# Performance work log

Hardware: AMD Instinct MI355X
Metric: run time of the kernel (lower is better)

The kernel has to match this reference:

```python
import jax, jax.numpy as jnp
import numpy as np

LOG_SQRT_2PI = 0.5 * float(np.log(2.0 * np.pi))  # 0.5*log(2*pi)


def _bayes_layer(x, mu, p, eps):
    # std_w = 1e-6 + softplus(W_p); W = W_mu + std_w * eps
    std = 1e-6 + jax.nn.softplus(p)
    W = mu + std * eps
    out = x @ W
    # variational posterior loglike q(W | mu, std), summed
    lqw = jnp.sum(-LOG_SQRT_2PI - jnp.log(std) - 0.5 * ((W - mu) / std) ** 2)
    # prior loglike N(0, 1) on detached W (original does W.detach().cpu().numpy())
    Wd = jax.lax.stop_gradient(W)
    lpw = jnp.sum(-LOG_SQRT_2PI - 0.5 * Wd ** 2)
    return out, lqw, lpw


def setup_inputs() -> dict:
    key = jax.random.key(0)
    ks = jax.random.split(key, 10)
    B, D_in, D_h, D_out = 65536, 512, 512, 10
    u = lambda k, s, lo, hi: jax.random.uniform(k, s, jnp.float32, lo, hi)
    return {
        "x": jax.random.normal(ks[0], (B, D_in), jnp.float32),
        "W_mu1": u(ks[1], (D_in, D_h), -0.2, 0.2),
        "W_p1": u(ks[2], (D_in, D_h), -3.0, -2.0),
        "eps1": jax.random.normal(ks[3], (D_in, D_h), jnp.float32),
        "W_mu2": u(ks[4], (D_h, D_h), -0.2, 0.2),
        "W_p2": u(ks[5], (D_h, D_h), -3.0, -2.0),
        "eps2": jax.random.normal(ks[6], (D_h, D_h), jnp.float32),
        "W_mu3": u(ks[7], (D_h, D_out), -0.2, 0.2),
        "W_p3": u(ks[8], (D_h, D_out), -3.0, -2.0),
        "eps3": jax.random.normal(ks[9], (D_h, D_out), jnp.float32),
    }


def reference(x, W_mu1, W_p1, eps1, W_mu2, W_p2, eps2, W_mu3, W_p3, eps3):
    # training / sample=True path of bayes_linear_2L.forward
    h, lqw1, lpw1 = _bayes_layer(x, W_mu1, W_p1, eps1)
    h = jax.nn.relu(h)
    h, lqw2, lpw2 = _bayes_layer(h, W_mu2, W_p2, eps2)
    h = jax.nn.relu(h)
    y, lqw3, lpw3 = _bayes_layer(h, W_mu3, W_p3, eps3)
    tlqw = lqw1 + lqw2 + lqw3
    tlpw = lpw1 + lpw2 + lpw3
    return (y, tlqw, tlpw)
```

## Files before the change

### kernel.cpp

```cpp
#include <hip/hip_runtime.h>
#include <hip/hip_bf16.h>
#include <stdint.h>

typedef unsigned char u8;
typedef unsigned int u32;
typedef long i64;
typedef i64 i64x2 __attribute__((ext_vector_type(2)));
typedef float f32x4 __attribute__((ext_vector_type(4)));

#define LOGSQRT2PI 0.9189385332046727f
#define SB0() __builtin_amdgcn_sched_barrier(0)
#define MFMA8(A, B, C) __builtin_amdgcn_mfma_f32_16x16x32_fp8_fp8(A, B, C, 0, 0, 0)

__device__ __forceinline__ void gload_lds16(const void* g, void* l) {
    __builtin_amdgcn_global_load_lds((__attribute__((address_space(1))) void*)g,
                                     (__attribute__((address_space(3))) void*)l,
                                     16, 0, 0);
}

__device__ __forceinline__ u8 to_fp8(float v) {
    return (u8)(__builtin_amdgcn_cvt_pk_fp8_f32(v, 0.f, 0, false) & 0xff);
}

__device__ __forceinline__ void prep_body(const float* __restrict__ mu,
        const float* __restrict__ p, const float* __restrict__ eps,
        u8* __restrict__ Wt, int N, int Npad, float* __restrict__ osc,
        int vb, int nblocks) {
    int total = 512 * Npad;
    float lqw = 0.f, lpw = 0.f;
    for (int idx = vb * 256 + threadIdx.x; idx < total; idx += nblocks * 256) {
        int k = idx / Npad, n = idx - k * Npad;
        float w = 0.f;
        if (n < N) {
            int src = k * N + n;
            float m = mu[src], e = eps[src];
            float sd = 1e-6f + log1pf(expf(p[src]));
            w = m + sd * e;
            float z = (w - m) / sd;
            lqw += -LOGSQRT2PI - logf(sd) - 0.5f * z * z;
            lpw += -LOGSQRT2PI - 0.5f * w * w;
        }
        Wt[n * 512 + k] = to_fp8(w);
    }
    #pragma unroll
    for (int off = 32; off; off >>= 1) {
        lqw += __shfl_down(lqw, off);
        lpw += __shfl_down(lpw, off);
    }
    if ((threadIdx.x & 63) == 0) {
        atomicAdd(&osc[0], lqw);
        atomicAdd(&osc[1], lpw);
    }
}

__global__ void k_prep_all(const float* __restrict__ mu1, const float* __restrict__ p1,
                           const float* __restrict__ e1,
                           const float* __restrict__ mu2, const float* __restrict__ p2,
                           const float* __restrict__ e2,
                           const float* __restrict__ mu3, const float* __restrict__ p3,
                           const float* __restrict__ e3,
                           u8* __restrict__ Wt1, u8* __restrict__ Wt2,
                           u8* __restrict__ Wt3, float* __restrict__ osc) {
    int b = blockIdx.x;
    if (b < 256)      prep_body(mu1, p1, e1, Wt1, 512, 512, osc, b, 256);
    else if (b < 512) prep_body(mu2, p2, e2, Wt2, 512, 512, osc, b - 256, 256);
    else              prep_body(mu3, p3, e3, Wt3, 10,  16,  osc, b - 512, 16);
}

__global__ void k_cvt8(const float4* __restrict__ in, uint2* __restrict__ out, int n8) {
    int stride = gridDim.x * blockDim.x;
    for (int i = blockIdx.x * blockDim.x + threadIdx.x; i < n8; i += stride) {
        float4 a = in[2 * i], b = in[2 * i + 1];
        u32 lo = __builtin_amdgcn_cvt_pk_fp8_f32(a.x, a.y, 0, false);
        lo = __builtin_amdgcn_cvt_pk_fp8_f32(a.z, a.w, (int)lo, true);
        u32 hi = __builtin_amdgcn_cvt_pk_fp8_f32(b.x, b.y, 0, false);
        hi = __builtin_amdgcn_cvt_pk_fp8_f32(b.z, b.w, (int)hi, true);
        out[i] = make_uint2(lo, hi);
    }
}

__global__ __launch_bounds__(256, 2)
void k_f8(const u8* __restrict__ xb, const u8* __restrict__ W1t,
          const u8* __restrict__ W2t, const u8* __restrict__ W3t,
          float* __restrict__ Y) {
    __shared__ __align__(16) u8 L[81920];
    const int tid = threadIdx.x;
    const int l = tid & 63, w = tid >> 6;
    const int r = l & 15, kq = l >> 4;
    const int l16 = l * 16;
    const long m0 = (long)blockIdx.x * 128 + w * 32;
    u8* scr = &L[65536 + w * 4096];

    #define STAGEW(WT, NT) { _Pragma("unroll")                                 \
        for (int i = 0; i < 16; i++) {                                         \
            const int c = w * 16 + i;                                          \
            gload_lds16((WT) + ((NT) * 128 + (c & 7) * 16 + r) * 512           \
                              + (c >> 3) * 64 + kq * 16,                       \
                        &L[c * 1024 + l16]);                                   \
        } }

    #define GLOOP(XF, ACC) { _Pragma("unroll")                                 \
        for (int kt = 0; kt < 8; kt++)                                         \
            _Pragma("unroll")                                                  \
            for (int jg = 0; jg < 8; jg++) {                                   \
                i64x2 bfr = *(const i64x2*)&L[(kt * 8 + jg) * 1024 + l16];     \
                ACC[jg] = MFMA8(XF[kt].x, bfr.x, ACC[jg]);                     \
                ACC[jg] = MFMA8(XF[kt].y, bfr.y, ACC[jg]);                     \
            } }

    #define TOSCR(ACC, RH) { _Pragma("unroll")                                 \
        for (int jg = 0; jg < 8; jg++)                                         \
            _Pragma("unroll")                                                  \
            for (int q = 0; q < 4; q++) {                                      \
                int row = (RH) * 16 + kq * 4 + q;                              \
                scr[row * 128 + ((jg ^ (row & 7)) << 4) + r] =                 \
                    to_fp8(fmaxf(ACC[jg][q], 0.f));                            \
            } }

    i64x2 xfA[8], xfB[8];
    #pragma unroll
    for (int kt = 0; kt < 8; kt++) {
        xfA[kt] = *(const i64x2*)(xb + (m0 + r) * 512 + kt * 64 + kq * 16);
        xfB[kt] = *(const i64x2*)(xb + (m0 + 16 + r) * 512 + kt * 64 + kq * 16);
    }

    i64x2 h1fA[8], h1fB[8];
    f32x4 yA = (f32x4){0.f, 0.f, 0.f, 0.f};
    f32x4 yB = (f32x4){0.f, 0.f, 0.f, 0.f};
    f32x4 acc[8];

    #pragma unroll 1
    for (int nt = 0; nt < 4; nt++) {
        STAGEW(W1t, nt);
        asm volatile("s_waitcnt vmcnt(0)" ::: "memory");
        __builtin_amdgcn_s_barrier();
        #pragma unroll
        for (int jg = 0; jg < 8; jg++) acc[jg] = (f32x4){0.f, 0.f, 0.f, 0.f};
        GLOOP(xfA, acc);
        TOSCR(acc, 0);
        #pragma unroll
        for (int jg = 0; jg < 8; jg++) acc[jg] = (f32x4){0.f, 0.f, 0.f, 0.f};
        GLOOP(xfB, acc);
        TOSCR(acc, 1);
        __builtin_amdgcn_s_barrier();
        asm volatile("s_waitcnt lgkmcnt(0)" ::: "memory");
        SB0();
        #pragma unroll
        for (int t2 = 0; t2 < 2; t2++) {
            h1fA[nt * 2 + t2] = *(const i64x2*)
                &scr[r * 128 + (((t2 * 4 + kq) ^ (r & 7)) << 4)];
            h1fB[nt * 2 + t2] = *(const i64x2*)
                &scr[(16 + r) * 128 + (((t2 * 4 + kq) ^ (r & 7)) << 4)];
        }
        asm volatile("s_waitcnt lgkmcnt(0)" ::: "memory");
        SB0();
    }

    #pragma unroll 1
    for (int nt = 0; nt < 4; nt++) {
        STAGEW(W2t, nt);
        asm volatile("s_waitcnt vmcnt(0)" ::: "memory");
        __builtin_amdgcn_s_barrier();
        #pragma unroll
        for (int jg = 0; jg < 8; jg++) acc[jg] = (f32x4){0.f, 0.f, 0.f, 0.f};
        GLOOP(h1fA, acc);
        TOSCR(acc, 0);
        #pragma unroll
        for (int jg = 0; jg < 8; jg++) acc[jg] = (f32x4){0.f, 0.f, 0.f, 0.f};
        GLOOP(h1fB, acc);
        TOSCR(acc, 1);
        __builtin_amdgcn_s_barrier();
        asm volatile("s_waitcnt lgkmcnt(0)" ::: "memory");
        SB0();
        #pragma unroll
        for (int t2 = 0; t2 < 2; t2++) {
            i64x2 a3A = *(const i64x2*)
                &scr[r * 128 + (((t2 * 4 + kq) ^ (r & 7)) << 4)];
            i64x2 a3B = *(const i64x2*)
                &scr[(16 + r) * 128 + (((t2 * 4 + kq) ^ (r & 7)) << 4)];
            i64x2 w3 = *(const i64x2*)(W3t + r * 512 + nt * 128 + t2 * 64 + kq * 16);
            yA = MFMA8(a3A.x, w3.x, yA);
            yA = MFMA8(a3A.y, w3.y, yA);
            yB = MFMA8(a3B.x, w3.x, yB);
            yB = MFMA8(a3B.y, w3.y, yB);
        }
        asm volatile("s_waitcnt lgkmcnt(0)" ::: "memory");
        SB0();
    }

    if (r < 10) {
        #pragma unroll
        for (int q = 0; q < 4; q++) {
            Y[(m0 + kq * 4 + q) * 10 + r]      = yA[q];
            Y[(m0 + 16 + kq * 4 + q) * 10 + r] = yB[q];
        }
    }
    #undef STAGEW
    #undef GLOOP
    #undef TOSCR
}

extern "C" void kernel_launch(void* const* d_in, const int* in_sizes, int n_in,
                              void* d_out, int out_size, void* d_ws, size_t ws_size,
                              hipStream_t stream) {
    const float* x   = (const float*)d_in[0];
    const float* mu1 = (const float*)d_in[1];
    const float* p1  = (const float*)d_in[2];
    const float* e1  = (const float*)d_in[3];
    const float* mu2 = (const float*)d_in[4];
    const float* p2  = (const float*)d_in[5];
    const float* e2  = (const float*)d_in[6];
    const float* mu3 = (const float*)d_in[7];
    const float* p3  = (const float*)d_in[8];
    const float* e3  = (const float*)d_in[9];
    float* out = (float*)d_out;

    const int B = 65536, D = 512, DO = 10;

    char* ws = (char*)d_ws;
    u8* Wt1 = (u8*)(ws);
    u8* Wt2 = (u8*)(ws + 262144);
    u8* Wt3 = (u8*)(ws + 524288);
    u8* xb  = (u8*)(ws + 1048576);

    float* osc = out + (long)B * DO;

    hipMemsetAsync(osc, 0, 2 * sizeof(float), stream);
    hipLaunchKernelGGL(k_prep_all, dim3(528), dim3(256), 0, stream,
                       mu1, p1, e1, mu2, p2, e2, mu3, p3, e3, Wt1, Wt2, Wt3, osc);
    hipLaunchKernelGGL(k_cvt8, dim3(2048), dim3(256), 0, stream,
                       (const float4*)x, (uint2*)xb, B * D / 8);
    hipLaunchKernelGGL(k_f8, dim3(512), dim3(256), 0, stream,
                       xb, Wt1, Wt2, Wt3, out);
}
```

Baseline: 165.0 us.

## Fuse x fp8 conversion into GEMM kernel and double-buffer weight tiles

Drops the separate x-to-fp8 conversion kernel. The main kernel now loads fp32 x directly and converts each fragment in registers, which removes a full write and re-read of the 32MB fp8 copy of x plus one launch. Weight staging is reworked into 64-column tiles double-buffered in LDS, so the next tile's global-to-LDS load overlaps the current tile's MFMAs, and both row halves share each B fragment read. The costs are more loop iterations and barriers, and higher register pressure while the fp32 x loads are in flight.

Result: faster. 138.4 us (-16.1%).

```diff
diff --git a/kernel.cpp b/kernel.cpp
--- a/kernel.cpp
+++ b/kernel.cpp
@@ -4,6 +4,7 @@
 
 typedef unsigned char u8;
 typedef unsigned int u32;
+typedef unsigned long long u64;
 typedef long i64;
 typedef i64 i64x2 __attribute__((ext_vector_type(2)));
 typedef float f32x4 __attribute__((ext_vector_type(4)));
@@ -20,6 +21,25 @@
 
 __device__ __forceinline__ u8 to_fp8(float v) {
     return (u8)(__builtin_amdgcn_cvt_pk_fp8_f32(v, 0.f, 0, false) & 0xff);
+}
+
+__device__ __forceinline__ i64x2 cvt_frag(const float* base) {
+    float4 v0 = *(const float4*)(base);
+    float4 v1 = *(const float4*)(base + 4);
+    float4 v2 = *(const float4*)(base + 8);
+    float4 v3 = *(const float4*)(base + 12);
+    u32 w0 = __builtin_amdgcn_cvt_pk_fp8_f32(v0.x, v0.y, 0, false);
+    w0 = __builtin_amdgcn_cvt_pk_fp8_f32(v0.z, v0.w, (int)w0, true);
+    u32 w1 = __builtin_amdgcn_cvt_pk_fp8_f32(v1.x, v1.y, 0, false);
+    w1 = __builtin_amdgcn_cvt_pk_fp8_f32(v1.z, v1.w, (int)w1, true);
+    u32 w2 = __builtin_amdgcn_cvt_pk_fp8_f32(v2.x, v2.y, 0, false);
+    w2 = __builtin_amdgcn_cvt_pk_fp8_f32(v2.z, v2.w, (int)w2, true);
+    u32 w3 = __builtin_amdgcn_cvt_pk_fp8_f32(v3.x, v3.y, 0, false);
+    w3 = __builtin_amdgcn_cvt_pk_fp8_f32(v3.z, v3.w, (int)w3, true);
+    i64x2 rr;
+    rr.x = (i64)(((u64)w1 << 32) | (u64)w0);
+    rr.y = (i64)(((u64)w3 << 32) | (u64)w2);
+    return rr;
 }
 
 __device__ __forceinline__ void prep_body(const float* __restrict__ mu,
@@ -67,20 +87,8 @@
     else              prep_body(mu3, p3, e3, Wt3, 10,  16,  osc, b - 512, 16);
 }
 
-__global__ void k_cvt8(const float4* __restrict__ in, uint2* __restrict__ out, int n8) {
-    int stride = gridDim.x * blockDim.x;
-    for (int i = blockIdx.x * blockDim.x + threadIdx.x; i < n8; i += stride) {
-        float4 a = in[2 * i], b = in[2 * i + 1];
-        u32 lo = __builtin_amdgcn_cvt_pk_fp8_f32(a.x, a.y, 0, false);
-        lo = __builtin_amdgcn_cvt_pk_fp8_f32(a.z, a.w, (int)lo, true);
-        u32 hi = __builtin_amdgcn_cvt_pk_fp8_f32(b.x, b.y, 0, false);
-        hi = __builtin_amdgcn_cvt_pk_fp8_f32(b.z, b.w, (int)hi, true);
-        out[i] = make_uint2(lo, hi);
-    }
-}
-
 __global__ __launch_bounds__(256, 2)
-void k_f8(const u8* __restrict__ xb, const u8* __restrict__ W1t,
+void k_f8(const float* __restrict__ X, const u8* __restrict__ W1t,
           const u8* __restrict__ W2t, const u8* __restrict__ W3t,
           float* __restrict__ Y) {
     __shared__ __align__(16) u8 L[81920];
@@ -91,94 +99,89 @@
     const long m0 = (long)blockIdx.x * 128 + w * 32;
     u8* scr = &L[65536 + w * 4096];
 
-    #define STAGEW(WT, NT) { _Pragma("unroll")                                 \
-        for (int i = 0; i < 16; i++) {                                         \
-            const int c = w * 16 + i;                                          \
-            gload_lds16((WT) + ((NT) * 128 + (c & 7) * 16 + r) * 512           \
-                              + (c >> 3) * 64 + kq * 16,                       \
-                        &L[c * 1024 + l16]);                                   \
+    #define STAGEW(WT, NT, BUF) { _Pragma("unroll")                            \
+        for (int i = 0; i < 8; i++) {                                          \
+            const int c = w * 8 + i;                                           \
+            const int jg = c & 3, kt = c >> 2;                                 \
+            gload_lds16((WT) + ((NT) * 64 + jg * 16 + r) * 512 + kt * 64 + kq * 16, \
+                        &L[(BUF) * 32768 + c * 1024 + l16]);                   \
         } }
 
-    #define GLOOP(XF, ACC) { _Pragma("unroll")                                 \
+    #define GLOOP(BUF, XA, XB) { _Pragma("unroll")                             \
         for (int kt = 0; kt < 8; kt++)                                         \
             _Pragma("unroll")                                                  \
-            for (int jg = 0; jg < 8; jg++) {                                   \
-                i64x2 bfr = *(const i64x2*)&L[(kt * 8 + jg) * 1024 + l16];     \
-                ACC[jg] = MFMA8(XF[kt].x, bfr.x, ACC[jg]);                     \
-                ACC[jg] = MFMA8(XF[kt].y, bfr.y, ACC[jg]);                     \
+            for (int jg = 0; jg < 4; jg++) {                                   \
+                i64x2 bfr = *(const i64x2*)&L[(BUF) * 32768 + (kt * 4 + jg) * 1024 + l16]; \
+                accA[jg] = MFMA8(XA[kt].x, bfr.x, accA[jg]);                   \
+                accA[jg] = MFMA8(XA[kt].y, bfr.y, accA[jg]);                   \
+                accB[jg] = MFMA8(XB[kt].x, bfr.x, accB[jg]);                   \
+                accB[jg] = MFMA8(XB[kt].y, bfr.y, accB[jg]);                   \
             } }
 
-    #define TOSCR(ACC, RH) { _Pragma("unroll")                                 \
-        for (int jg = 0; jg < 8; jg++)                                         \
+    #define TOSCR() { _Pragma("unroll")                                        \
+        for (int jg = 0; jg < 4; jg++)                                         \
             _Pragma("unroll")                                                  \
             for (int q = 0; q < 4; q++) {                                      \
-                int row = (RH) * 16 + kq * 4 + q;                              \
-                scr[row * 128 + ((jg ^ (row & 7)) << 4) + r] =                 \
-                    to_fp8(fmaxf(ACC[jg][q], 0.f));                            \
+                int rowA = kq * 4 + q;                                         \
+                int rowB = 16 + kq * 4 + q;                                    \
+                scr[rowA * 128 + ((jg ^ (rowA & 7)) << 4) + r] =               \
+                    to_fp8(fmaxf(accA[jg][q], 0.f));                           \
+                scr[rowB * 128 + ((jg ^ (rowB & 7)) << 4) + r] =               \
+                    to_fp8(fmaxf(accB[jg][q], 0.f));                           \
             } }
 
+    #define ZACC() { _Pragma("unroll")                                         \
+        for (int jg = 0; jg < 4; jg++) {                                       \
+            accA[jg] = (f32x4){0.f, 0.f, 0.f, 0.f};                            \
+            accB[jg] = (f32x4){0.f, 0.f, 0.f, 0.f};                            \
+        } }
+
+    f32x4 accA[4], accB[4];
     i64x2 xfA[8], xfB[8];
-    #pragma unroll
-    for (int kt = 0; kt < 8; kt++) {
-        xfA[kt] = *(const i64x2*)(xb + (m0 + r) * 512 + kt * 64 + kq * 16);
-        xfB[kt] = *(const i64x2*)(xb + (m0 + 16 + r) * 512 + kt * 64 + kq * 16);
-    }
-
     i64x2 h1fA[8], h1fB[8];
     f32x4 yA = (f32x4){0.f, 0.f, 0.f, 0.f};
     f32x4 yB = (f32x4){0.f, 0.f, 0.f, 0.f};
-    f32x4 acc[8];
+
+    STAGEW(W1t, 0, 0);
+    #pragma unroll
+    for (int kt = 0; kt < 8; kt++) {
+        xfA[kt] = cvt_frag(X + (m0 + r) * 512 + kt * 64 + kq * 16);
+        xfB[kt] = cvt_frag(X + (m0 + 16 + r) * 512 + kt * 64 + kq * 16);
+    }
+    asm volatile("s_waitcnt vmcnt(0)" ::: "memory");
+    __builtin_amdgcn_s_barrier();
 
     #pragma unroll 1
-    for (int nt = 0; nt < 4; nt++) {
-        STAGEW(W1t, nt);
+    for (int nt = 0; nt < 8; nt++) {
+        const int buf = nt & 1;
+        if (nt < 7) { STAGEW(W1t, nt + 1, buf ^ 1); }
+        else        { STAGEW(W2t, 0, buf ^ 1); }
+        ZACC();
+        GLOOP(buf, xfA, xfB);
+        TOSCR();
+        asm volatile("s_waitcnt lgkmcnt(0)" ::: "memory");
+        SB0();
+        h1fA[nt] = *(const i64x2*)&scr[r * 128 + ((kq ^ (r & 7)) << 4)];
+        h1fB[nt] = *(const i64x2*)&scr[(16 + r) * 128 + ((kq ^ (r & 7)) << 4)];
+        asm volatile("s_waitcnt lgkmcnt(0)" ::: "memory");
+        SB0();
         asm volatile("s_waitcnt vmcnt(0)" ::: "memory");
         __builtin_amdgcn_s_barrier();
-        #pragma unroll
-        for (int jg = 0; jg < 8; jg++) acc[jg] = (f32x4){0.f, 0.f, 0.f, 0.f};
-        GLOOP(xfA, acc);
-        TOSCR(acc, 0);
-        #pragma unroll
-        for (int jg = 0; jg < 8; jg++) acc[jg] = (f32x4){0.f, 0.f, 0.f, 0.f};
-        GLOOP(xfB, acc);
-        TOSCR(acc, 1);
-        __builtin_amdgcn_s_barrier();
-        asm volatile("s_waitcnt lgkmcnt(0)" ::: "memory");
-        SB0();
-        #pragma unroll
-        for (int t2 = 0; t2 < 2; t2++) {
-            h1fA[nt * 2 + t2] = *(const i64x2*)
-                &scr[r * 128 + (((t2 * 4 + kq) ^ (r & 7)) << 4)];
-            h1fB[nt * 2 + t2] = *(const i64x2*)
-                &scr[(16 + r) * 128 + (((t2 * 4 + kq) ^ (r & 7)) << 4)];
-        }
-        asm volatile("s_waitcnt lgkmcnt(0)" ::: "memory");
-        SB0();
     }
 
     #pragma unroll 1
-    for (int nt = 0; nt < 4; nt++) {
-        STAGEW(W2t, nt);
-        asm volatile("s_waitcnt vmcnt(0)" ::: "memory");
-        __builtin_amdgcn_s_barrier();
-        #pragma unroll
-        for (int jg = 0; jg < 8; jg++) acc[jg] = (f32x4){0.f, 0.f, 0.f, 0.f};
-        GLOOP(h1fA, acc);
-        TOSCR(acc, 0);
-        #pragma unroll
-        for (int jg = 0; jg < 8; jg++) acc[jg] = (f32x4){0.f, 0.f, 0.f, 0.f};
-        GLOOP(h1fB, acc);
-        TOSCR(acc, 1);
-        __builtin_amdgcn_s_barrier();
-        asm volatile("s_waitcnt lgkmcnt(0)" ::: "memory");
-        SB0();
-        #pragma unroll
-        for (int t2 = 0; t2 < 2; t2++) {
-            i64x2 a3A = *(const i64x2*)
-                &scr[r * 128 + (((t2 * 4 + kq) ^ (r & 7)) << 4)];
-            i64x2 a3B = *(const i64x2*)
-                &scr[(16 + r) * 128 + (((t2 * 4 + kq) ^ (r & 7)) << 4)];
-            i64x2 w3 = *(const i64x2*)(W3t + r * 512 + nt * 128 + t2 * 64 + kq * 16);
+    for (int nt = 0; nt < 8; nt++) {
+        const int buf = (nt + 1) & 1;
+        if (nt < 7) STAGEW(W2t, nt + 1, buf ^ 1);
+        ZACC();
+        GLOOP(buf, h1fA, h1fB);
+        TOSCR();
+        asm volatile("s_waitcnt lgkmcnt(0)" ::: "memory");
+        SB0();
+        {
+            i64x2 a3A = *(const i64x2*)&scr[r * 128 + ((kq ^ (r & 7)) << 4)];
+            i64x2 a3B = *(const i64x2*)&scr[(16 + r) * 128 + ((kq ^ (r & 7)) << 4)];
+            i64x2 w3 = *(const i64x2*)(W3t + r * 512 + nt * 64 + kq * 16);
             yA = MFMA8(a3A.x, w3.x, yA);
             yA = MFMA8(a3A.y, w3.y, yA);
             yB = MFMA8(a3B.x, w3.x, yB);
@@ -186,6 +189,8 @@
         }
         asm volatile("s_waitcnt lgkmcnt(0)" ::: "memory");
         SB0();
+        if (nt < 7) { asm volatile("s_waitcnt vmcnt(0)" ::: "memory"); }
+        __builtin_amdgcn_s_barrier();
     }
 
     if (r < 10) {
@@ -198,6 +203,7 @@
     #undef STAGEW
     #undef GLOOP
     #undef TOSCR
+    #undef ZACC
 }
 
 extern "C" void kernel_launch(void* const* d_in, const int* in_sizes, int n_in,
@@ -215,21 +221,18 @@
     const float* e3  = (const float*)d_in[9];
     float* out = (float*)d_out;
 
-    const int B = 65536, D = 512, DO = 10;
+    const int B = 65536, DO = 10;
 
     char* ws = (char*)d_ws;
     u8* Wt1 = (u8*)(ws);
     u8* Wt2 = (u8*)(ws + 262144);
     u8* Wt3 = (u8*)(ws + 524288);
-    u8* xb  = (u8*)(ws + 1048576);
 
     float* osc = out + (long)B * DO;
 
     hipMemsetAsync(osc, 0, 2 * sizeof(float), stream);
     hipLaunchKernelGGL(k_prep_all, dim3(528), dim3(256), 0, stream,
                        mu1, p1, e1, mu2, p2, e2, mu3, p3, e3, Wt1, Wt2, Wt3, osc);
-    hipLaunchKernelGGL(k_cvt8, dim3(2048), dim3(256), 0, stream,
-                       (const float4*)x, (uint2*)xb, B * D / 8);
     hipLaunchKernelGGL(k_f8, dim3(512), dim3(256), 0, stream,
-                       xb, Wt1, Wt2, Wt3, out);
-}
+                       x, Wt1, Wt2, Wt3, out);
+}
```
